# Optimization experiments

Measured on AMD Instinct MI355X. Metric: run time of the kernel, lower is better.

Reference implementation:

```python
import jax, jax.numpy as jnp
import numpy as np

Q_LEN = 2048
K_LEN = 2048
BATCH = 2
EMBED = 1024
HEADS = 16
HEAD_DIM = EMBED // HEADS
PE_ROWS = 2 * K_LEN


def _shift(p):
    # Transformer-XL pad/flatten shift: p is [B, H, Q, S] with S = 2*K-1 -> [B, H, Q, K]
    B, H, Q, S = p.shape
    pp = jnp.pad(p, ((0, 0), (0, 0), (0, 1), (0, 1)))          # [B,H,Q+1,S+1]
    flat = pp.reshape(B, H, (Q + 1) * (S + 1))
    flat = jax.lax.slice_in_dim(flat, S // 2, S // 2 + Q * S, axis=-1)
    return flat.reshape(B, H, Q, S)[..., : (S + 1) // 2]


def setup_inputs() -> dict:
    key = jax.random.key(0)
    ks = jax.random.split(key, 11)
    ws = 0.02  # weight scale
    inp = {
        "query": jax.random.normal(ks[0], (Q_LEN, BATCH, EMBED), jnp.float32),
        "key": jax.random.normal(ks[1], (K_LEN, BATCH, EMBED), jnp.float32),
        "value": jax.random.normal(ks[2], (K_LEN, BATCH, EMBED), jnp.float32),
        "pe": jax.random.normal(ks[3], (PE_ROWS, EMBED), jnp.float32),
        "w_q": jax.random.normal(ks[4], (EMBED, EMBED), jnp.float32) * ws,
        "w_k": jax.random.normal(ks[5], (EMBED, EMBED), jnp.float32) * ws,
        "w_v": jax.random.normal(ks[6], (EMBED, EMBED), jnp.float32) * ws,
        "w_k_pos": jax.random.normal(ks[7], (EMBED, EMBED), jnp.float32) * ws,
        "out_proj": jax.random.normal(ks[8], (EMBED, EMBED), jnp.float32) * ws,
        "content_bias": jax.random.normal(ks[9], (HEADS, HEAD_DIM), jnp.float32) * ws,
        "pos_bias": jax.random.normal(ks[10], (HEADS, HEAD_DIM), jnp.float32) * ws,
        "attn_mask": jnp.triu(jnp.ones((Q_LEN, K_LEN), dtype=bool), k=1),  # causal
    }
    return inp


def reference(query, key, value, pe, w_q, w_k, w_v, w_k_pos, out_proj,
              content_bias, pos_bias, attn_mask):
    Qlen, B, E = query.shape
    Klen = key.shape[0]
    H, D = content_bias.shape
    scaling = D ** -0.5

    # projections (torch Linear: x @ W^T); layout -> [B, H, L, D]
    q = (query @ w_q.T).reshape(Qlen, B, H, D).transpose(1, 2, 0, 3)
    k = (key @ w_k.T).reshape(Klen, B, H, D).transpose(1, 2, 0, 3)
    v = (value @ w_v.T).reshape(Klen, B, H, D).transpose(1, 2, 0, 3)

    # relative position keys: pe slice of size 2K-1 starting at pe.size(0)//2 - K + 1
    lower = pe.shape[0] // 2 - Klen + 1
    pe_slice = jax.lax.dynamic_slice_in_dim(pe, lower, 2 * Klen - 1, axis=0)
    k_pos = (pe_slice @ w_k_pos.T).reshape(2 * Klen - 1, H, D).transpose(1, 0, 2)  # [H, 2K-1, D]

    content = jnp.einsum('bhqd,bhkd->bhqk', q + content_bias[None, :, None, :], k)
    pos = jnp.einsum('bhqd,hsd->bhqs', q + pos_bias[None, :, None, :], k_pos)
    pos = _shift(pos)  # [B, H, Q, K]

    attn = (content + pos) * scaling
    attn = jnp.where(attn_mask[None, None], -jnp.inf, attn)
    w = jax.nn.softmax(attn, axis=-1)

    out = jnp.einsum('bhqk,bhkd->bhqd', w, v)
    out = out.transpose(2, 0, 1, 3).reshape(Qlen, B, E)
    return out @ out_proj.T
```

## Files before the change

kernel.cpp:

```cpp
#include <hip/hip_runtime.h>
#include <hip/hip_bf16.h>

typedef __hip_bfloat16 bf16;
typedef __attribute__((ext_vector_type(8))) short short8;
typedef __attribute__((ext_vector_type(8))) unsigned short u16x8;
typedef __attribute__((ext_vector_type(4))) float f32x4;

#define QL   2048
#define KLEN 2048
#define BATCH 2
#define EMB  1024
#define NH   16
#define HD   64
#define SPE  4095

__device__ __forceinline__ int detect_f32_wave(const void* __restrict__ p) {
    const ushort4 v = ((const ushort4*)p)[threadIdx.x & 63];
    int c = 0;
    c += __popcll(__ballot(((v.x >> 7) & 0xFF) >= 0x8A));
    c += __popcll(__ballot(((v.y >> 7) & 0xFF) >= 0x8A));
    c += __popcll(__ballot(((v.z >> 7) & 0xFF) >= 0x8A));
    c += __popcll(__ballot(((v.w >> 7) & 0xFF) >= 0x8A));
    return c >= 8;
}

__device__ __forceinline__ ushort4 cvt4(const void* src, long u4i, int f32) {
    ushort4 o;
    if (f32) {
        float4 v = ((const float4*)src)[u4i];
        bf16 a = (bf16)v.x, b = (bf16)v.y, c = (bf16)v.z, e = (bf16)v.w;
        o.x = *(unsigned short*)&a; o.y = *(unsigned short*)&b;
        o.z = *(unsigned short*)&c; o.w = *(unsigned short*)&e;
    } else {
        o = ((const ushort4*)src)[u4i];
    }
    return o;
}

__global__ __launch_bounds__(256) void conv_all(
    const void* w0, const void* w1, const void* w2, const void* w3, const void* w4,
    const void* cb, const void* pb, bf16* __restrict__ wdst,
    const void* q, const void* k, const void* v, const void* pe,
    bf16* __restrict__ dq, bf16* __restrict__ dk,
    bf16* __restrict__ dv, bf16* __restrict__ dp)
{
    const int t = threadIdx.x;
    const int bid = blockIdx.x;
    __shared__ int f32s;
    if (bid < 1280) {
        const int seg = bid >> 8, inner = bid & 255;
        const void* src = seg == 0 ? w0 : seg == 1 ? w1 : seg == 2 ? w2 : seg == 3 ? w3 : w4;
        bf16* d = wdst + (size_t)seg * 1048576;
        if (t < 64) { int r = detect_f32_wave(src); if (t == 0) f32s = r; }
        __syncthreads();
        const int f32 = f32s;
#pragma unroll
        for (int i = 0; i < 4; i++) {
            long u4i = (long)inner * 1024 + i * 256 + t;
            ((ushort4*)d)[u4i] = cvt4(src, u4i, f32);
        }
    } else if (bid == 1280) {
        if (t < 64) { int r = detect_f32_wave(cb); if (t == 0) f32s = r; }
        __syncthreads();
        const int f32 = f32s;
        ((ushort4*)(wdst + 5242880))[t]        = cvt4(cb, t, f32);
        ((ushort4*)(wdst + 5242880 + 1024))[t] = cvt4(pb, t, f32);
    } else {
        const int abid = bid - 1281;
        const int seg = abid >> 10, inner = abid & 1023;
        const void* src = seg == 0 ? q : seg == 1 ? k : seg == 2 ? v : pe;
        bf16* d = seg == 0 ? dq : seg == 1 ? dk : seg == 2 ? dv : dp;
        const long srcOff4 = (seg == 3) ? 256 : 0;
        const long zero4   = (seg == 3) ? 1048320 : (1L << 40);
        if (t < 64) { int r = detect_f32_wave(src); if (t == 0) f32s = r; }
        __syncthreads();
        const int f32 = f32s;
#pragma unroll
        for (int i = 0; i < 4; i++) {
            long u4i = (long)inner * 1024 + i * 256 + t;
            ushort4 o;
            if (u4i >= zero4) { o.x = o.y = o.z = o.w = 0; }
            else o = cvt4(src, srcOff4 + u4i, f32);
            ((ushort4*)d)[u4i] = o;
        }
    }
}

__device__ __forceinline__ void llds16(const bf16* g, bf16* l) {
    __builtin_amdgcn_global_load_lds(
        (const __attribute__((address_space(1))) void*)g,
        (__attribute__((address_space(3))) void*)l,
        16, 0, 0);
}

__global__ __launch_bounds__(256, 2) void gemm_big(
    const bf16* __restrict__ A0, const bf16* __restrict__ A1,
    const bf16* __restrict__ A2, const bf16* __restrict__ A3,
    const bf16* __restrict__ wslab,
    bf16* __restrict__ qc, bf16* __restrict__ qp,
    bf16* __restrict__ kw, bf16* __restrict__ vw,
    bf16* __restrict__ kpos, float* __restrict__ outf, int mode_base)
{
    const int o = blockIdx.x;
    const int mode = mode_base + (o >> 7);
    const int s = (o >> 3) & 15;
    const int bx = (o & 7) + 8 * (s & 3);
    const int by = s >> 2;

    const bf16* A = mode == 0 ? A0 : mode == 1 ? A1 : mode == 2 ? A2 : A3;
    const bf16* W = wslab + (size_t)mode * 1048576;

    __shared__ __align__(16) bf16 Asd[3][128 * 32];
    __shared__ __align__(16) bf16 Wsd[3][256 * 32];

    const int t = threadIdx.x;
    const int w = t >> 6, lane = t & 63, lm = lane & 15, quad = lane >> 4;
    const int m0 = bx * 128, n0 = by * 256;
    const int wr = (w >> 1) * 64, wc = (w & 1) * 128;

    f32x4 acc[4][8] = {};

    auto stage = [&](int buf, int k0) {
#pragma unroll
        for (int i = 0; i < 2; i++) {
            int c = i * 256 + t, r = c >> 2, ch = c & 3, gc = ch ^ (r & 3);
            llds16(A + (size_t)(m0 + r) * 1024 + k0 + gc * 8, Asd[buf] + (c & ~63) * 8);
        }
#pragma unroll
        for (int i = 0; i < 4; i++) {
            int c = i * 256 + t, r = c >> 2, ch = c & 3, gc = ch ^ (r & 3);
            llds16(W + (size_t)(n0 + r) * 1024 + k0 + gc * 8, Wsd[buf] + (c & ~63) * 8);
        }
    };

    stage(0, 0);
    stage(1, 32);
    int cur = 0, sb = 2;
    for (int it = 0; it < 32; ++it) {
        if (it == 31) asm volatile("s_waitcnt vmcnt(0) lgkmcnt(0)" ::: "memory");
        else          asm volatile("s_waitcnt vmcnt(6) lgkmcnt(0)" ::: "memory");
        __builtin_amdgcn_s_barrier();
        __builtin_amdgcn_sched_barrier(0);
        if (it < 30) stage(sb, (it + 2) * 32);

        short8 af[4], wf[8];
#pragma unroll
        for (int x = 0; x < 4; x++) {
            int ra = wr + x * 16 + lm;
            af[x] = *(const short8*)&Asd[cur][ra * 32 + ((quad ^ (ra & 3)) * 8)];
        }
#pragma unroll
        for (int y = 0; y < 8; y++) {
            int rb = wc + y * 16 + lm;
            wf[y] = *(const short8*)&Wsd[cur][rb * 32 + ((quad ^ (rb & 3)) * 8)];
        }
#pragma unroll
        for (int mt = 0; mt < 4; mt++)
#pragma unroll
            for (int nt = 0; nt < 8; nt++)
                acc[mt][nt] = __builtin_amdgcn_mfma_f32_16x16x32_bf16(
                    af[mt], wf[nt], acc[mt][nt], 0, 0, 0);

        cur = cur == 2 ? 0 : cur + 1;
        sb  = sb  == 2 ? 0 : sb + 1;
    }

    const bf16* cbb = wslab + 5242880;
    const bf16* pbb = wslab + 5242880 + 1024;

#pragma unroll
    for (int mt = 0; mt < 4; mt++) {
#pragma unroll
        for (int nt = 0; nt < 8; nt++) {
#pragma unroll
            for (int r4 = 0; r4 < 4; r4++) {
                int row = m0 + wr + mt * 16 + quad * 4 + r4;
                int col = n0 + wc + nt * 16 + lm;
                float v = acc[mt][nt][r4];
                if (mode == 0) {
                    int l = row >> 1, b = row & 1;
                    int h = col >> 6, d = col & 63;
                    size_t idx = ((size_t)(b * NH + h) * QL + l) * HD + d;
                    qc[idx] = (bf16)(v + __bfloat162float(cbb[col]));
                    qp[idx] = (bf16)(v + __bfloat162float(pbb[col]));
                } else if (mode == 1) {
                    int l = row >> 1, b = row & 1;
                    int h = col >> 6, d = col & 63;
                    kw[((size_t)(b * NH + h) * KLEN + l) * HD + d] = (bf16)v;
                } else if (mode == 2) {
                    int l = row >> 1, b = row & 1;
                    int h = col >> 6, d = col & 63;
                    vw[((size_t)(b * NH + h) * KLEN + l) * HD + d] = (bf16)v;
                } else if (mode == 3) {
                    if (row < SPE) {
                        int h = col >> 6, d = col & 63;
                        kpos[((size_t)h * SPE + row) * HD + d] = (bf16)v;
                    }
                } else {
                    outf[(size_t)row * 1024 + col] = v;
                }
            }
        }
    }
}

#define NEG_INF (-1.0e30f)
#define SCL2 0.18033688011f

__global__ __launch_bounds__(256) void attn_mfma(
    const bf16* __restrict__ qc_g, const bf16* __restrict__ qp_g,
    const bf16* __restrict__ k_g,  const bf16* __restrict__ v_g,
    const bf16* __restrict__ kpos_g, bf16* __restrict__ ao)
{
    const int lin = blockIdx.x + (blockIdx.y << 6) + (blockIdx.z << 10);
    const int xcd = lin & 7, s = lin >> 3;
    const int g   = (xcd << 2) | (s >> 6);
    const int u   = s & 63;
    const int bx  = 63 - u;
    const int h   = g & 15;
    const int b   = g >> 4;
    const int q0  = bx * 32;

    const bf16* qc_bh  = qc_g + ((size_t)(b * NH + h) * QL) * HD;
    const bf16* qp_bh  = qp_g + ((size_t)(b * NH + h) * QL) * HD;
    const bf16* k_bh   = k_g  + ((size_t)(b * NH + h) * KLEN) * HD;
    const bf16* v_bh   = v_g  + ((size_t)(b * NH + h) * KLEN) * HD;
    const bf16* kpos_h = kpos_g + (size_t)h * SPE * HD;

    __shared__ __align__(16) bf16 K_s [64 * 64];
    __shared__ __align__(16) bf16 Kp_s[96 * 64];
    __shared__ __align__(16) bf16 Vt_s[64 * 64];
    __shared__ __align__(16) bf16 Pb_s[32 * 64];
    __shared__ float Sc_s[32][69];
    __shared__ float Pt_s[32][98];
    __shared__ float arow_s[32];

    const int t = threadIdx.x;
    const int w = t >> 6, lane = t & 63, lm = lane & 15, quad = lane >> 4;

    const int sr = t >> 3;
    const int sc = (t & 7) * 8;
    const int vrr = t >> 3, vch = t & 7;
    const int vkc = vrr >> 2;

    const int mtc = w & 1;
    const int ntc = (w >> 1) * 2;
    const int mtp = w >> 1;
    const int ntp = (w & 1) * 3;

    float m_run = NEG_INF, l_part = 0.0f;
    f32x4 accO[2] = {{0,0,0,0},{0,0,0,0}};
    u16x8 vv0, vv1;

    const int nkt = (bx >> 1) + 1;

    short8 aQc0, aQc1, aQp0, aQp1;
    {
        const bf16* qr = qc_bh + (size_t)(q0 + mtc * 16 + lm) * HD;
        aQc0 = *(const short8*)(qr + quad * 8);
        aQc1 = *(const short8*)(qr + (4 + quad) * 8);
        const bf16* pr = qp_bh + (size_t)(q0 + mtp * 16 + lm) * HD;
        aQp0 = *(const short8*)(pr + quad * 8);
        aQp1 = *(const short8*)(pr + (4 + quad) * 8);
    }

#pragma unroll
    for (int i = 0; i < 2; i++) {
        int c = i * 256 + t, r = c >> 3, ch = c & 7, gc = ch ^ (r & 7);
        llds16(k_bh + (size_t)r * HD + gc * 8, K_s + (c & ~63) * 8);
    }
    {
        const int s0 = 2016 - q0;
#pragma unroll
        for (int i = 0; i < 3; i++) {
            int c = i * 256 + t, r = c >> 3, ch = c & 7, gc = ch ^ (r & 7);
            llds16(kpos_h + (size_t)(s0 + r) * HD + gc * 8, Kp_s + (c & ~63) * 8);
        }
    }
    vv0 = *(const u16x8*)&v_bh[(size_t)(2 * vrr)     * HD + vch * 8];
    vv1 = *(const u16x8*)&v_bh[(size_t)(2 * vrr + 1) * HD + vch * 8];

    for (int kt = 0; kt < nkt; kt++) {
        const int k0 = kt * 64;

        __syncthreads();

        {
            const int off = (2 * vrr) & 7;
#pragma unroll
            for (int j = 0; j < 8; j++) {
                unsigned int pair = (unsigned int)vv0[j] | ((unsigned int)vv1[j] << 16);
                int slot = vkc ^ vch ^ j;
                *(unsigned int*)&Vt_s[(vch * 8 + j) * 64 + slot * 8 + off] = pair;
            }
        }

        {
#pragma unroll
            for (int n = 0; n < 2; n++) {
                int rowB = (ntc + n) * 16 + lm;
                short8 b0 = *(const short8*)&K_s[rowB * 64 + ((quad)     ^ (rowB & 7)) * 8];
                short8 b1 = *(const short8*)&K_s[rowB * 64 + ((4 + quad) ^ (rowB & 7)) * 8];
                f32x4 acc = {0, 0, 0, 0};
                acc = __builtin_amdgcn_mfma_f32_16x16x32_bf16(aQc0, b0, acc, 0, 0, 0);
                acc = __builtin_amdgcn_mfma_f32_16x16x32_bf16(aQc1, b1, acc, 0, 0, 0);
#pragma unroll
                for (int r = 0; r < 4; r++)
                    Sc_s[mtc * 16 + quad * 4 + r][(ntc + n) * 16 + lm] = acc[r];
            }
        }
        {
#pragma unroll
            for (int n = 0; n < 3; n++) {
                int rowB = (ntp + n) * 16 + lm;
                short8 b0 = *(const short8*)&Kp_s[rowB * 64 + ((quad)     ^ (rowB & 7)) * 8];
                short8 b1 = *(const short8*)&Kp_s[rowB * 64 + ((4 + quad) ^ (rowB & 7)) * 8];
                f32x4 acc = {0, 0, 0, 0};
                acc = __builtin_amdgcn_mfma_f32_16x16x32_bf16(aQp0, b0, acc, 0, 0, 0);
                acc = __builtin_amdgcn_mfma_f32_16x16x32_bf16(aQp1, b1, acc, 0, 0, 0);
#pragma unroll
                for (int r = 0; r < 4; r++)
                    Pt_s[mtp * 16 + quad * 4 + r][(ntp + n) * 16 + lm] = acc[r];
            }
        }

        __syncthreads();

        if (kt + 1 < nkt) {
            const int k0n = k0 + 64;
            const int s0n = k0n - q0 + 2016;
#pragma unroll
            for (int i = 0; i < 2; i++) {
                int c = i * 256 + t, r = c >> 3, ch = c & 7, gc = ch ^ (r & 7);
                llds16(k_bh + (size_t)(k0n + r) * HD + gc * 8, K_s + (c & ~63) * 8);
            }
#pragma unroll
            for (int i = 0; i < 3; i++) {
                int c = i * 256 + t, r = c >> 3, ch = c & 7, gc = ch ^ (r & 7);
                llds16(kpos_h + (size_t)(s0n + r) * HD + gc * 8, Kp_s + (c & ~63) * 8);
            }
            vv0 = *(const u16x8*)&v_bh[(size_t)(k0n + 2 * vrr)     * HD + vch * 8];
            vv1 = *(const u16x8*)&v_bh[(size_t)(k0n + 2 * vrr + 1) * HD + vch * 8];
        }

        {
            float p[8];
            float pmax = NEG_INF;
#pragma unroll
            for (int j = 0; j < 8; j++) {
                int col = sc + j;
                float sv = (Sc_s[sr][col] + Pt_s[sr][col - sr + 31]) * SCL2;
                if (k0 + col > q0 + sr) sv = NEG_INF;
                p[j] = sv;
                pmax = fmaxf(pmax, sv);
            }
            float alpha = 1.0f;
            if (!__all(pmax <= m_run + 11.5f)) {
                float mx = pmax;
                mx = fmaxf(mx, __shfl_xor(mx, 1, 8));
                mx = fmaxf(mx, __shfl_xor(mx, 2, 8));
                mx = fmaxf(mx, __shfl_xor(mx, 4, 8));
                float mnew = fmaxf(m_run, mx);
                alpha = __builtin_amdgcn_exp2f(m_run - mnew);
                m_run = mnew;
            }
            float ls = 0.0f;
#pragma unroll
            for (int j = 0; j < 8; j++) {
                p[j] = __builtin_amdgcn_exp2f(p[j] - m_run);
                ls += p[j];
            }
            l_part = l_part * alpha + ls;
            if ((t & 7) == 0) arow_s[sr] = alpha;
            short8 pv;
#pragma unroll
            for (int j = 0; j < 8; j++) { bf16 x = (bf16)p[j]; pv[j] = *(short*)&x; }
            *(short8*)&Pb_s[sr * 64 + ((t & 7) ^ (sr & 7)) * 8] = pv;
        }

        asm volatile("s_waitcnt lgkmcnt(0)" ::: "memory");
        __builtin_amdgcn_s_barrier();
        __builtin_amdgcn_sched_barrier(0);

        {
            float al[4];
#pragma unroll
            for (int r = 0; r < 4; r++) al[r] = arow_s[mtc * 16 + quad * 4 + r];
            int rowA = mtc * 16 + lm;
            short8 a0 = *(const short8*)&Pb_s[rowA * 64 + ((quad)     ^ (rowA & 7)) * 8];
            short8 a1 = *(const short8*)&Pb_s[rowA * 64 + ((4 + quad) ^ (rowA & 7)) * 8];
#pragma unroll
            for (int n = 0; n < 2; n++) {
                int d = (ntc + n) * 16 + lm;
                int ds = (d >> 3) ^ (d & 7);
                short8 b0 = *(const short8*)&Vt_s[d * 64 + ((quad     ^ ds)) * 8];
                short8 b1 = *(const short8*)&Vt_s[d * 64 + (((4 + quad) ^ ds)) * 8];
#pragma unroll
                for (int r = 0; r < 4; r++) accO[n][r] *= al[r];
                accO[n] = __builtin_amdgcn_mfma_f32_16x16x32_bf16(a0, b0, accO[n], 0, 0, 0);
                accO[n] = __builtin_amdgcn_mfma_f32_16x16x32_bf16(a1, b1, accO[n], 0, 0, 0);
            }
        }
    }

    l_part += __shfl_xor(l_part, 1, 8);
    l_part += __shfl_xor(l_part, 2, 8);
    l_part += __shfl_xor(l_part, 4, 8);

    __syncthreads();
    if ((t & 7) == 0) arow_s[sr] = l_part;
    __syncthreads();

    float linv[4];
#pragma unroll
    for (int r = 0; r < 4; r++) linv[r] = 1.0f / arow_s[mtc * 16 + quad * 4 + r];
#pragma unroll
    for (int n = 0; n < 2; n++) {
#pragma unroll
        for (int r = 0; r < 4; r++) {
            int row = mtc * 16 + quad * 4 + r;
            ao[(((size_t)(q0 + row) * BATCH + b) * EMB) + h * HD + (ntc + n) * 16 + lm] =
                (bf16)(accO[n][r] * linv[r]);
        }
    }
}

extern "C" void kernel_launch(void* const* d_in, const int* in_sizes, int n_in,
                              void* d_out, int out_size, void* d_ws, size_t ws_size,
                              hipStream_t stream)
{
    const void* query = d_in[0];
    const void* key   = d_in[1];
    const void* value = d_in[2];
    const void* pe    = d_in[3];
    const void* w_q   = d_in[4];
    const void* w_k   = d_in[5];
    const void* w_v   = d_in[6];
    const void* w_kp  = d_in[7];
    const void* w_out = d_in[8];
    const void* cb    = d_in[9];
    const void* pb    = d_in[10];
    float* out = (float*)d_out;

    const size_t SLAB = 4194304;
    bf16* qc   = (bf16*)d_ws;
    bf16* qp   = qc + SLAB;
    bf16* kw   = qp + SLAB;
    bf16* vw   = kw + SLAB;
    bf16* kpos = vw + SLAB;
    bf16* ao   = kpos + SLAB;
    bf16* stg  = ao + SLAB;
    bf16* wqb  = stg + SLAB;

    bf16* stgQ = (bf16*)d_out;
    bf16* stgV = stgQ + SLAB;

    dim3 blk(256);

    conv_all<<<dim3(5377), blk, 0, stream>>>(
        w_q, w_k, w_v, w_kp, w_out, cb, pb, wqb,
        query, key, value, pe, stgQ, stg, stgV, ao);

    gemm_big<<<dim3(512), blk, 0, stream>>>(
        stgQ, stg, stgV, ao, wqb, qc, qp, kw, vw, kpos, nullptr, 0);

    attn_mfma<<<dim3(64, NH, BATCH), blk, 0, stream>>>(qc, qp, kw, vw, kpos, ao);

    gemm_big<<<dim3(128), blk, 0, stream>>>(
        stgQ, stg, stgV, ao, wqb, qc, qp, kw, vw, kpos, out, 4);
}
```

Measured before the change: 363.9 us.

## Fuse fp32-to-bf16 activation conversion into projection GEMM A-tile staging

Drops the separate pass that converted query/key/value/pe activations to bf16 staging buffers. The projection GEMM now loads fp32 A tiles into registers, converts them to bf16 and writes them to LDS. This removes a full read-write round trip over about 64MB of activations. In exchange the A path no longer uses direct global-to-LDS loads and drops from triple to double buffering with extra barriers, which may expose more load latency in the GEMM mainloop.

After: 355.6 us. 1.02x faster.

```diff
diff --git a/kernel.cpp b/kernel.cpp
--- a/kernel.cpp
+++ b/kernel.cpp
@@ -37,12 +37,9 @@
     return o;
 }
 
-__global__ __launch_bounds__(256) void conv_all(
+__global__ __launch_bounds__(256) void conv_w(
     const void* w0, const void* w1, const void* w2, const void* w3, const void* w4,
-    const void* cb, const void* pb, bf16* __restrict__ wdst,
-    const void* q, const void* k, const void* v, const void* pe,
-    bf16* __restrict__ dq, bf16* __restrict__ dk,
-    bf16* __restrict__ dv, bf16* __restrict__ dp)
+    const void* cb, const void* pb, bf16* __restrict__ wdst)
 {
     const int t = threadIdx.x;
     const int bid = blockIdx.x;
@@ -59,30 +56,12 @@
             long u4i = (long)inner * 1024 + i * 256 + t;
             ((ushort4*)d)[u4i] = cvt4(src, u4i, f32);
         }
-    } else if (bid == 1280) {
+    } else {
         if (t < 64) { int r = detect_f32_wave(cb); if (t == 0) f32s = r; }
         __syncthreads();
         const int f32 = f32s;
         ((ushort4*)(wdst + 5242880))[t]        = cvt4(cb, t, f32);
         ((ushort4*)(wdst + 5242880 + 1024))[t] = cvt4(pb, t, f32);
-    } else {
-        const int abid = bid - 1281;
-        const int seg = abid >> 10, inner = abid & 1023;
-        const void* src = seg == 0 ? q : seg == 1 ? k : seg == 2 ? v : pe;
-        bf16* d = seg == 0 ? dq : seg == 1 ? dk : seg == 2 ? dv : dp;
-        const long srcOff4 = (seg == 3) ? 256 : 0;
-        const long zero4   = (seg == 3) ? 1048320 : (1L << 40);
-        if (t < 64) { int r = detect_f32_wave(src); if (t == 0) f32s = r; }
-        __syncthreads();
-        const int f32 = f32s;
-#pragma unroll
-        for (int i = 0; i < 4; i++) {
-            long u4i = (long)inner * 1024 + i * 256 + t;
-            ushort4 o;
-            if (u4i >= zero4) { o.x = o.y = o.z = o.w = 0; }
-            else o = cvt4(src, srcOff4 + u4i, f32);
-            ((ushort4*)d)[u4i] = o;
-        }
     }
 }
 
@@ -93,10 +72,122 @@
         16, 0, 0);
 }
 
+__device__ __forceinline__ short8 pack_f32x8(const float4& a, const float4& b) {
+    short8 o; bf16 x;
+    x = (bf16)a.x; o[0] = *(short*)&x;  x = (bf16)a.y; o[1] = *(short*)&x;
+    x = (bf16)a.z; o[2] = *(short*)&x;  x = (bf16)a.w; o[3] = *(short*)&x;
+    x = (bf16)b.x; o[4] = *(short*)&x;  x = (bf16)b.y; o[5] = *(short*)&x;
+    x = (bf16)b.z; o[6] = *(short*)&x;  x = (bf16)b.w; o[7] = *(short*)&x;
+    return o;
+}
+
+template<bool F32>
+struct AStage {
+    u16x8  u[2];
+    float4 f[2][2];
+    __device__ __forceinline__ void load(const void* Av, const int go[2], int k0) {
+#pragma unroll
+        for (int i = 0; i < 2; i++) {
+            int e = go[i] + k0;
+            if (F32) {
+                const float4* F = (const float4*)Av;
+                f[i][0] = F[e >> 2];
+                f[i][1] = F[(e >> 2) + 1];
+            } else {
+                u[i] = ((const u16x8*)Av)[e >> 3];
+            }
+        }
+    }
+    __device__ __forceinline__ void write(bf16* dst, int t) {
+#pragma unroll
+        for (int i = 0; i < 2; i++) {
+            int c = i * 256 + t;
+            short8 v;
+            if (F32) v = pack_f32x8(f[i][0], f[i][1]);
+            else     v = *(short8*)&u[i];
+            *(short8*)&dst[c * 8] = v;
+        }
+    }
+};
+
+__device__ __forceinline__ void gcompute(
+    const bf16* As, const bf16* Ws, int wr, int wc, int lm, int quad,
+    f32x4 acc[4][8])
+{
+    short8 af[4], wf[8];
+#pragma unroll
+    for (int x = 0; x < 4; x++) {
+        int ra = wr + x * 16 + lm;
+        af[x] = *(const short8*)&As[ra * 32 + ((quad ^ (ra & 3)) * 8)];
+    }
+#pragma unroll
+    for (int y = 0; y < 8; y++) {
+        int rb = wc + y * 16 + lm;
+        wf[y] = *(const short8*)&Ws[rb * 32 + ((quad ^ (rb & 3)) * 8)];
+    }
+#pragma unroll
+    for (int mt = 0; mt < 4; mt++)
+#pragma unroll
+        for (int nt = 0; nt < 8; nt++)
+            acc[mt][nt] = __builtin_amdgcn_mfma_f32_16x16x32_bf16(
+                af[mt], wf[nt], acc[mt][nt], 0, 0, 0);
+}
+
+#define GWB() do { asm volatile("s_waitcnt vmcnt(0) lgkmcnt(0)" ::: "memory"); \
+    __builtin_amdgcn_s_barrier(); __builtin_amdgcn_sched_barrier(0); } while (0)
+#define GLB() do { asm volatile("s_waitcnt lgkmcnt(0)" ::: "memory"); \
+    __builtin_amdgcn_s_barrier(); __builtin_amdgcn_sched_barrier(0); } while (0)
+
+template<bool F32>
+__device__ void gloop(
+    const void* Av, const bf16* W, int m0, int n0, int mode,
+    bf16* Asd0, bf16* Asd1, bf16* Wsd0, bf16* Wsd1,
+    int t, int wr, int wc, int lm, int quad, f32x4 acc[4][8])
+{
+    int go[2];
+#pragma unroll
+    for (int i = 0; i < 2; i++) {
+        int c = i * 256 + t, r = c >> 2, gc = (c & 3) ^ (r & 3);
+        int ar = m0 + r;
+        if (mode == 3) { ar = ar + 1; if (ar > 4095) ar = 4095; }
+        go[i] = ar * 1024 + gc * 8;
+    }
+    auto stageW = [&](bf16* dst, int k0) {
+#pragma unroll
+        for (int i = 0; i < 4; i++) {
+            int c = i * 256 + t, r = c >> 2, gc = (c & 3) ^ (r & 3);
+            llds16(W + (size_t)(n0 + r) * 1024 + k0 + gc * 8, dst + (c & ~63) * 8);
+        }
+    };
+
+    AStage<F32> sa, sb;
+    sa.load(Av, go, 0);
+    stageW(Wsd0, 0);
+
+#pragma unroll 1
+    for (int tt = 0; tt < 32; tt += 2) {
+        GWB();
+        sa.write(Asd0, t);
+        GLB();
+        sb.load(Av, go, (tt + 1) * 32);
+        stageW(Wsd1, (tt + 1) * 32);
+        gcompute(Asd0, Wsd0, wr, wc, lm, quad, acc);
+
+        GWB();
+        sb.write(Asd1, t);
+        GLB();
+        if (tt + 2 < 32) {
+            sa.load(Av, go, (tt + 2) * 32);
+            stageW(Wsd0, (tt + 2) * 32);
+        }
+        gcompute(Asd1, Wsd1, wr, wc, lm, quad, acc);
+    }
+}
+
 __global__ __launch_bounds__(256, 2) void gemm_big(
-    const bf16* __restrict__ A0, const bf16* __restrict__ A1,
-    const bf16* __restrict__ A2, const bf16* __restrict__ A3,
-    const bf16* __restrict__ wslab,
+    const void* __restrict__ Aq, const void* __restrict__ Ak,
+    const void* __restrict__ Avv, const void* __restrict__ Ape,
+    const bf16* __restrict__ ao, const bf16* __restrict__ wslab,
     bf16* __restrict__ qc, bf16* __restrict__ qp,
     bf16* __restrict__ kw, bf16* __restrict__ vw,
     bf16* __restrict__ kpos, float* __restrict__ outf, int mode_base)
@@ -107,63 +198,28 @@
     const int bx = (o & 7) + 8 * (s & 3);
     const int by = s >> 2;
 
-    const bf16* A = mode == 0 ? A0 : mode == 1 ? A1 : mode == 2 ? A2 : A3;
+    const void* A = mode == 0 ? Aq : mode == 1 ? Ak : mode == 2 ? Avv :
+                    mode == 3 ? Ape : (const void*)ao;
     const bf16* W = wslab + (size_t)mode * 1048576;
 
-    __shared__ __align__(16) bf16 Asd[3][128 * 32];
-    __shared__ __align__(16) bf16 Wsd[3][256 * 32];
+    __shared__ __align__(16) bf16 Asd[2][128 * 32];
+    __shared__ __align__(16) bf16 Wsd[2][256 * 32];
+    __shared__ int f32s;
 
     const int t = threadIdx.x;
     const int w = t >> 6, lane = t & 63, lm = lane & 15, quad = lane >> 4;
     const int m0 = bx * 128, n0 = by * 256;
     const int wr = (w >> 1) * 64, wc = (w & 1) * 128;
 
+    if (t < 64) { int r = detect_f32_wave(A); if (t == 0) f32s = r; }
+    __syncthreads();
+
     f32x4 acc[4][8] = {};
 
-    auto stage = [&](int buf, int k0) {
-#pragma unroll
-        for (int i = 0; i < 2; i++) {
-            int c = i * 256 + t, r = c >> 2, ch = c & 3, gc = ch ^ (r & 3);
-            llds16(A + (size_t)(m0 + r) * 1024 + k0 + gc * 8, Asd[buf] + (c & ~63) * 8);
-        }
-#pragma unroll
-        for (int i = 0; i < 4; i++) {
-            int c = i * 256 + t, r = c >> 2, ch = c & 3, gc = ch ^ (r & 3);
-            llds16(W + (size_t)(n0 + r) * 1024 + k0 + gc * 8, Wsd[buf] + (c & ~63) * 8);
-        }
-    };
-
-    stage(0, 0);
-    stage(1, 32);
-    int cur = 0, sb = 2;
-    for (int it = 0; it < 32; ++it) {
-        if (it == 31) asm volatile("s_waitcnt vmcnt(0) lgkmcnt(0)" ::: "memory");
-        else          asm volatile("s_waitcnt vmcnt(6) lgkmcnt(0)" ::: "memory");
-        __builtin_amdgcn_s_barrier();
-        __builtin_amdgcn_sched_barrier(0);
-        if (it < 30) stage(sb, (it + 2) * 32);
-
-        short8 af[4], wf[8];
-#pragma unroll
-        for (int x = 0; x < 4; x++) {
-            int ra = wr + x * 16 + lm;
-            af[x] = *(const short8*)&Asd[cur][ra * 32 + ((quad ^ (ra & 3)) * 8)];
-        }
-#pragma unroll
-        for (int y = 0; y < 8; y++) {
-            int rb = wc + y * 16 + lm;
-            wf[y] = *(const short8*)&Wsd[cur][rb * 32 + ((quad ^ (rb & 3)) * 8)];
-        }
-#pragma unroll
-        for (int mt = 0; mt < 4; mt++)
-#pragma unroll
-            for (int nt = 0; nt < 8; nt++)
-                acc[mt][nt] = __builtin_amdgcn_mfma_f32_16x16x32_bf16(
-                    af[mt], wf[nt], acc[mt][nt], 0, 0, 0);
-
-        cur = cur == 2 ? 0 : cur + 1;
-        sb  = sb  == 2 ? 0 : sb + 1;
-    }
+    if (f32s) gloop<true >(A, W, m0, n0, mode, Asd[0], Asd[1], Wsd[0], Wsd[1],
+                           t, wr, wc, lm, quad, acc);
+    else      gloop<false>(A, W, m0, n0, mode, Asd[0], Asd[1], Wsd[0], Wsd[1],
+                           t, wr, wc, lm, quad, acc);
 
     const bf16* cbb = wslab + 5242880;
     const bf16* pbb = wslab + 5242880 + 1024;
@@ -449,23 +505,17 @@
     bf16* vw   = kw + SLAB;
     bf16* kpos = vw + SLAB;
     bf16* ao   = kpos + SLAB;
-    bf16* stg  = ao + SLAB;
-    bf16* wqb  = stg + SLAB;
-
-    bf16* stgQ = (bf16*)d_out;
-    bf16* stgV = stgQ + SLAB;
+    bf16* wqb  = ao + SLAB;
 
     dim3 blk(256);
 
-    conv_all<<<dim3(5377), blk, 0, stream>>>(
-        w_q, w_k, w_v, w_kp, w_out, cb, pb, wqb,
-        query, key, value, pe, stgQ, stg, stgV, ao);
+    conv_w<<<dim3(1281), blk, 0, stream>>>(w_q, w_k, w_v, w_kp, w_out, cb, pb, wqb);
 
     gemm_big<<<dim3(512), blk, 0, stream>>>(
-        stgQ, stg, stgV, ao, wqb, qc, qp, kw, vw, kpos, nullptr, 0);
+        query, key, value, pe, nullptr, wqb, qc, qp, kw, vw, kpos, nullptr, 0);
 
     attn_mfma<<<dim3(64, NH, BATCH), blk, 0, stream>>>(qc, qp, kw, vw, kpos, ao);
 
     gemm_big<<<dim3(128), blk, 0, stream>>>(
-        stgQ, stg, stgV, ao, wqb, qc, qp, kw, vw, kpos, out, 4);
-}
+        query, key, value, pe, ao, wqb, qc, qp, kw, vw, kpos, out, 4);
+}
```
